# Performance work log

Measured on AMD Instinct MI355X. Metric: run time of the kernel, lower is better.

The kernel has to match this reference:

```python
import jax, jax.numpy as jnp
import numpy as np

D_EMB = 256


def setup_inputs() -> dict:
    key = jax.random.key(0)
    ks = jax.random.split(key, 7)
    B, S, d = 4, 4096, D_EMB
    scale = 1.0 / np.sqrt(d)
    return {
        "x": jax.random.normal(ks[0], (B, S, d), jnp.float32),
        "Wqkv": jax.random.normal(ks[1], (d, 3 * d), jnp.float32) * scale,
        "bqkv": jax.random.normal(ks[2], (3 * d,), jnp.float32) * 0.02,
        "Wproj": jax.random.normal(ks[3], (d, d), jnp.float32) * scale,
        "bproj": jax.random.normal(ks[4], (d,), jnp.float32) * 0.02,
        "Wfc": jax.random.normal(ks[5], (d, 1), jnp.float32) * scale,
        "bfc": jax.random.normal(ks[6], (1,), jnp.float32) * 0.02,
    }


def reference(x, Wqkv, bqkv, Wproj, bproj, Wfc, bfc):
    # qkv projection: [B,S,3d] -> split into q,k,v [B,S,d]
    qkv = x @ Wqkv + bqkv
    q, k, v = jnp.split(qkv, 3, axis=2)
    # full attention scores [B,S,S]; note: original applies NO 1/sqrt(d)
    # scaling (dead branch in source), 'traditional' softmax over last dim
    attn_scores = jnp.einsum("bqd,bkd->bqk", q, k)
    attn_weights = jax.nn.softmax(attn_scores, axis=-1)
    y = jnp.einsum("bqk,bkd->bqd", attn_weights, v)
    y = y @ Wproj + bproj
    out = y @ Wfc + bfc  # [B,S,1]
    return out
```

## Files before the change

kernel.cpp:

```cpp
#include <hip/hip_runtime.h>
#include <hip/hip_bf16.h>

#define BQ 4
#define SQ 4096
#define DQ 256
#define N3 768
#define KBLK 64
#define NITER (SQ / KBLK)
#define KHALF (NITER / 2)
#define LOG2E 1.44269504f
#define THR2 11.5415603f

typedef __attribute__((ext_vector_type(8))) _Float16 f16x8;
typedef __attribute__((ext_vector_type(4))) float f32x4;
typedef __attribute__((ext_vector_type(4))) unsigned int u32x4;

__device__ __forceinline__ short f2h(float f) {
  _Float16 h = (_Float16)f;
  union { _Float16 h; short s; } v; v.h = h;
  return v.s;
}

__device__ __forceinline__ void gload16(const void* g, void* lds) {
  __builtin_amdgcn_global_load_lds(
      (const __attribute__((address_space(1))) unsigned int*)g,
      (__attribute__((address_space(3))) unsigned int*)lds, 16, 0, 0);
}

__global__ __launch_bounds__(256) void prep_kernel(
    const float* __restrict__ Wqkv, const float* __restrict__ Wproj,
    const float* __restrict__ bproj, const float* __restrict__ Wfc,
    const float* __restrict__ bfc, short* __restrict__ W16T,
    float* __restrict__ Wc) {
  const int t = threadIdx.x;
  if (blockIdx.x == 48) {
    __shared__ float wf[256];
    wf[t] = Wfc[t];
    __syncthreads();
    float acc = 0.f;
    for (int j = 0; j < 256; ++j) acc += Wproj[(size_t)t * 256 + j] * wf[j];
    Wc[t] = acc;
    if (t == 0) {
      float c = bfc[0];
      for (int j = 0; j < 256; ++j) c += bproj[j] * wf[j];
      Wc[256] = c;
    }
    return;
  }
  __shared__ float tile[64][65];
  const int nb = (blockIdx.x % 12) * 64;
  const int kb = (blockIdx.x / 12) * 64;
  const int tr = t >> 6, tc = t & 63;
#pragma unroll
  for (int i = 0; i < 16; ++i)
    tile[tr + i * 4][tc] = Wqkv[(size_t)(kb + tr + i * 4) * N3 + nb + tc];
  __syncthreads();
#pragma unroll
  for (int i = 0; i < 16; ++i)
    W16T[(size_t)(nb + tr + i * 4) * 256 + kb + tc] = f2h(tile[tc][tr + i * 4]);
}

__global__ __launch_bounds__(1024, 4) void qkv_kernel(
    const float* __restrict__ x, const short* __restrict__ W16T,
    const float* __restrict__ bqkv, const float* __restrict__ Wc,
    short* __restrict__ Qb, short* __restrict__ Kb, float* __restrict__ u) {
  __shared__ short xs[64][264];
  __shared__ short ws[2][64][256];
  __shared__ float u_red[4][4][16];
  const int t = threadIdx.x;
  const int l = t & 63, w = t >> 6;
  const int lr = l & 15, lg = l >> 4;
  const int mq = w >> 2, nq = w & 3;
  const int Mbase = blockIdx.x * 64;

#define STAGE_W(BUF, NT)                                                      \
  {                                                                           \
    _Pragma("unroll") for (int i = 0; i < 2; ++i) {                           \
      const int n = w * 4 + i * 2 + (l >> 5);                                 \
      const int gc = (l & 31) ^ (n & 7);                                      \
      gload16(W16T + (size_t)((NT)*64 + n) * 256 + gc * 8,                    \
              &ws[BUF][w * 4 + i * 2][0]);                                    \
    }                                                                         \
  }

  STAGE_W(0, 0);

  {
    const int m = t >> 4, kc = (t & 15) * 16;
    const float* src = x + (size_t)(Mbase + m) * DQ + kc;
    short tmp[16];
#pragma unroll
    for (int i = 0; i < 16; ++i) tmp[i] = f2h(src[i]);
    *(u32x4*)&xs[m][kc] = *(u32x4*)&tmp[0];
    *(u32x4*)&xs[m][kc + 8] = *(u32x4*)&tmp[8];
  }

  float bias_qk[8], bias_u[4], wc_u[4];
#pragma unroll
  for (int i = 0; i < 8; ++i) bias_qk[i] = bqkv[i * 64 + nq * 16 + lr];
#pragma unroll
  for (int i = 0; i < 4; ++i) {
    bias_u[i] = bqkv[512 + i * 64 + nq * 16 + lr];
    wc_u[i] = Wc[i * 64 + nq * 16 + lr];
  }

  __syncthreads();

  unsigned qksto[8][2];
  float upart[4] = {0.f, 0.f, 0.f, 0.f};

#pragma unroll
  for (int nt = 0; nt < 12; ++nt) {
    const int cur = nt & 1;
    if (nt + 1 < 12) {
      STAGE_W(cur ^ 1, nt + 1);
      asm volatile("s_waitcnt vmcnt(2)" ::: "memory");
    } else {
      asm volatile("s_waitcnt vmcnt(0)" ::: "memory");
    }
    __builtin_amdgcn_s_barrier();
    __builtin_amdgcn_sched_barrier(0);

    f32x4 acc = {};
    const char* wR = (const char*)&ws[cur][nq * 16 + lr][0];
#pragma unroll
    for (int kk = 0; kk < 8; ++kk) {
      f16x8 af = *(f16x8*)&xs[mq * 16 + lr][kk * 32 + lg * 8];
      f16x8 bfr = *(const f16x8*)(wR + (((4 * kk + lg) ^ (lr & 7)) << 4));
      acc = __builtin_amdgcn_mfma_f32_16x16x32_f16(af, bfr, acc, 0, 0, 0);
    }
    if (nt < 8) {
      const float sc = (nt < 4) ? 1.f : LOG2E;
      unsigned s0 = (unsigned short)f2h((acc[0] + bias_qk[nt]) * sc);
      unsigned s1 = (unsigned short)f2h((acc[1] + bias_qk[nt]) * sc);
      unsigned s2 = (unsigned short)f2h((acc[2] + bias_qk[nt]) * sc);
      unsigned s3 = (unsigned short)f2h((acc[3] + bias_qk[nt]) * sc);
      qksto[nt][0] = s0 | (s1 << 16);
      qksto[nt][1] = s2 | (s3 << 16);
    } else {
#pragma unroll
      for (int r = 0; r < 4; ++r) upart[r] += (acc[r] + bias_u[nt - 8]) * wc_u[nt - 8];
    }
    __builtin_amdgcn_s_barrier();
  }

#pragma unroll
  for (int nt = 0; nt < 8; ++nt) {
    const int col = nt * 64 + nq * 16 + lr;
#pragma unroll
    for (int r = 0; r < 4; ++r) {
      const int row = Mbase + mq * 16 + lg * 4 + r;
      const short sv = (short)((qksto[nt][r >> 1] >> ((r & 1) * 16)) & 0xFFFF);
      if (col < 256) Qb[(size_t)row * DQ + col] = sv;
      else           Kb[(size_t)row * DQ + (col - 256)] = sv;
    }
  }

#pragma unroll
  for (int mask = 1; mask <= 8; mask <<= 1)
#pragma unroll
    for (int r = 0; r < 4; ++r) upart[r] += __shfl_xor(upart[r], mask, 64);
  if (lr == 0) {
#pragma unroll
    for (int r = 0; r < 4; ++r) u_red[mq][nq][lg * 4 + r] = upart[r];
  }
  __syncthreads();
  if (t < 64)
    u[Mbase + t] = u_red[t >> 4][0][t & 15] + u_red[t >> 4][1][t & 15] +
                   u_red[t >> 4][2][t & 15] + u_red[t >> 4][3][t & 15];
#undef STAGE_W
}

__global__ __launch_bounds__(256, 2) void attn_kernel(
    const short* __restrict__ Qb, const short* __restrict__ Kb,
    const float* __restrict__ u, float* __restrict__ Pm,
    float* __restrict__ Pd, float* __restrict__ Pn) {
  __shared__ short Ks[2][64][256];
  __shared__ __align__(16) float u_lds[2048];
  __shared__ float Mrg[2][2][32][3];

  const int t = threadIdx.x;
  const int l = t & 63, w = t >> 6;
  const int lr = l & 15, lg = l >> 4;
  const int qg = w >> 1, h = w & 1;
  const int bid = blockIdx.x;
  const int b = bid & 3;
  const int half = (bid >> 2) & 1;
  const int qbase = (bid >> 3) * 64;

  const short* kbase = Kb + ((size_t)b * SQ + (size_t)half * (SQ / 2)) * DQ;
  const float* ubase = u + (size_t)b * SQ + half * (SQ / 2);

#define STAGE(BUF, KB)                                                      \
  {                                                                         \
    _Pragma("unroll") for (int i = 0; i < 8; ++i) {                         \
      const int kr = w * 16 + i * 2 + (l >> 5);                             \
      const int gc = (l & 31) ^ (kr & 7);                                   \
      gload16(kbase + (size_t)((KB)*64 + kr) * DQ + gc * 8,                 \
              &Ks[BUF][w * 16 + i * 2][0]);                                 \
    }                                                                       \
  }

  STAGE(0, 0);
  gload16(ubase + w * 256 + (l << 2), &u_lds[w * 256]);
  gload16(ubase + (4 + w) * 256 + (l << 2), &u_lds[(4 + w) * 256]);

  f16x8 qf[2][8];
#pragma unroll
  for (int mm = 0; mm < 2; ++mm) {
    const short* qptr = Qb + (size_t)(b * SQ + qbase + qg * 32 + mm * 16 + lr) * DQ;
#pragma unroll
    for (int kk = 0; kk < 8; ++kk)
      qf[mm][kk] = *(const f16x8*)(qptr + kk * 32 + lg * 8);
  }

  int koff[8];
#pragma unroll
  for (int kk = 0; kk < 8; ++kk) koff[kk] = ((4 * kk + lg) ^ (lr & 7)) << 4;

  float m_run[2] = {-1e30f, -1e30f};
  float num[2][2] = {}, den[2][2] = {};

  __syncthreads();

  for (int kb = 0; kb < KHALF; ++kb) {
    const int cur = kb & 1;
    if (kb + 1 < KHALF) {
      STAGE(cur ^ 1, kb + 1);
      asm volatile("s_waitcnt vmcnt(8)" ::: "memory");
    } else {
      asm volatile("s_waitcnt vmcnt(0)" ::: "memory");
    }
    __builtin_amdgcn_s_barrier();
    __builtin_amdgcn_sched_barrier(0);

    f32x4 uv[2];
#pragma unroll
    for (int kc = 0; kc < 2; ++kc)
      uv[kc] = *(const f32x4*)&u_lds[kb * 64 + h * 32 + kc * 16 + lg * 4];

    f16x8 kf[2][8];
#pragma unroll
    for (int kc = 0; kc < 2; ++kc) {
      const char* kR = (const char*)&Ks[cur][h * 32 + kc * 16 + lr][0];
#pragma unroll
      for (int kk = 0; kk < 8; ++kk)
        kf[kc][kk] = *(const f16x8*)(kR + koff[kk]);
    }

    f32x4 s[2][2] = {};
    __builtin_amdgcn_s_setprio(1);
#pragma unroll
    for (int kc = 0; kc < 2; ++kc)
#pragma unroll
      for (int kk = 0; kk < 8; ++kk) {
        s[kc][0] = __builtin_amdgcn_mfma_f32_16x16x32_f16(kf[kc][kk], qf[0][kk], s[kc][0], 0, 0, 0);
        s[kc][1] = __builtin_amdgcn_mfma_f32_16x16x32_f16(kf[kc][kk], qf[1][kk], s[kc][1], 0, 0, 0);
      }
    __builtin_amdgcn_s_setprio(0);

    float mx[2];
#pragma unroll
    for (int mm = 0; mm < 2; ++mm)
      mx[mm] = fmaxf(fmaxf(fmaxf(s[0][mm][0], s[0][mm][1]),
                           fmaxf(s[0][mm][2], s[0][mm][3])),
                     fmaxf(fmaxf(s[1][mm][0], s[1][mm][1]),
                           fmaxf(s[1][mm][2], s[1][mm][3])));
    const bool over = (mx[0] > m_run[0] + THR2) || (mx[1] > m_run[1] + THR2);
    if (__any(over)) {
#pragma unroll
      for (int mm = 0; mm < 2; ++mm) {
        float mt = mx[mm];
        mt = fmaxf(mt, __shfl_xor(mt, 16, 64));
        mt = fmaxf(mt, __shfl_xor(mt, 32, 64));
        const float mn = fmaxf(m_run[mm], mt);
        const float sc = __builtin_amdgcn_exp2f(m_run[mm] - mn);
        m_run[mm] = mn;
#pragma unroll
        for (int kc = 0; kc < 2; ++kc) { num[mm][kc] *= sc; den[mm][kc] *= sc; }
      }
    }
#pragma unroll
    for (int kc = 0; kc < 2; ++kc) {
#pragma unroll
      for (int mm = 0; mm < 2; ++mm)
#pragma unroll
        for (int r = 0; r < 4; ++r) {
          const float p = __builtin_amdgcn_exp2f(s[kc][mm][r] - m_run[mm]);
          den[mm][kc] += p;
          num[mm][kc] += p * uv[kc][r];
        }
    }
    __builtin_amdgcn_s_barrier();
  }

  float numt[2], dent[2];
#pragma unroll
  for (int mm = 0; mm < 2; ++mm) {
    numt[mm] = num[mm][0] + num[mm][1];
    dent[mm] = den[mm][0] + den[mm][1];
    numt[mm] += __shfl_xor(numt[mm], 16, 64);
    numt[mm] += __shfl_xor(numt[mm], 32, 64);
    dent[mm] += __shfl_xor(dent[mm], 16, 64);
    dent[mm] += __shfl_xor(dent[mm], 32, 64);
  }
  if (lg == 0) {
#pragma unroll
    for (int mm = 0; mm < 2; ++mm) {
      Mrg[qg][h][mm * 16 + lr][0] = m_run[mm];
      Mrg[qg][h][mm * 16 + lr][1] = dent[mm];
      Mrg[qg][h][mm * 16 + lr][2] = numt[mm];
    }
  }
  __syncthreads();

  if (t < 64) {
    const int row = t & 31, qg2 = t >> 5;
    const float m0 = Mrg[qg2][0][row][0], m1 = Mrg[qg2][1][row][0];
    const float M = fmaxf(m0, m1);
    const float e0 = __builtin_amdgcn_exp2f(m0 - M);
    const float e1 = __builtin_amdgcn_exp2f(m1 - M);
    const float dt = e0 * Mrg[qg2][0][row][1] + e1 * Mrg[qg2][1][row][1];
    const float nt = e0 * Mrg[qg2][0][row][2] + e1 * Mrg[qg2][1][row][2];
    const size_t idx = (size_t)half * (BQ * SQ) + (size_t)b * SQ + qbase + qg2 * 32 + row;
    Pm[idx] = M; Pd[idx] = dt; Pn[idx] = nt;
  }
#undef STAGE
}

__global__ void merge_kernel(const float* __restrict__ Pm,
                             const float* __restrict__ Pd,
                             const float* __restrict__ Pn,
                             const float* __restrict__ Wc,
                             float* __restrict__ out) {
  const int gid = blockIdx.x * 256 + threadIdx.x;
  const float m0 = Pm[gid], m1 = Pm[BQ * SQ + gid];
  const float M = fmaxf(m0, m1);
  const float e0 = __builtin_amdgcn_exp2f(m0 - M);
  const float e1 = __builtin_amdgcn_exp2f(m1 - M);
  const float den = e0 * Pd[gid] + e1 * Pd[BQ * SQ + gid];
  const float num = e0 * Pn[gid] + e1 * Pn[BQ * SQ + gid];
  out[gid] = num / den + Wc[256];
}

extern "C" void kernel_launch(void* const* d_in, const int* in_sizes, int n_in,
                              void* d_out, int out_size, void* d_ws, size_t ws_size,
                              hipStream_t stream) {
  const float* x     = (const float*)d_in[0];
  const float* Wqkv  = (const float*)d_in[1];
  const float* bqkv  = (const float*)d_in[2];
  const float* Wproj = (const float*)d_in[3];
  const float* bproj = (const float*)d_in[4];
  const float* Wfc   = (const float*)d_in[5];
  const float* bfc   = (const float*)d_in[6];
  float* out = (float*)d_out;

  const size_t SEG = (size_t)BQ * SQ * DQ * 2;
  char* wsb = (char*)d_ws;
  short* Qb   = (short*)(wsb);
  short* Kb   = (short*)(wsb + SEG);
  char* base  = wsb + 2 * SEG;
  float* Wc   = (float*)(base);
  float* u    = (float*)(base + 4096);
  short* W16T = (short*)(base + 4096 + 65536);
  float* Pm   = (float*)(base + 4096 + 65536 + 393216);
  float* Pd   = Pm + 2 * BQ * SQ;
  float* Pn   = Pd + 2 * BQ * SQ;

  prep_kernel<<<49, 256, 0, stream>>>(Wqkv, Wproj, bproj, Wfc, bfc, W16T, Wc);
  qkv_kernel<<<256, 1024, 0, stream>>>(x, W16T, bqkv, Wc, Qb, Kb, u);
  attn_kernel<<<512, 256, 0, stream>>>(Qb, Kb, u, Pm, Pd, Pn);
  merge_kernel<<<BQ * SQ / 256, 256, 0, stream>>>(Pm, Pd, Pn, Wc, out);
}
```

Before: 93.83 us.

## Load K fragments directly from global into registers, dropping LDS staging

Replaces the double-buffered LDS staging of K tiles with direct per-lane global loads into register fragments, software-pipelined so one 16-row chunk loads while MFMAs run on the other. This removes the LDS round trip and the per-iteration barriers. The cost is that the two waves sharing the same h, one per query group, each load the same K rows themselves, so global and L2 traffic for K doubles. It also adds register pressure, which may hurt occupancy at 2 blocks per CU.

```diff
diff --git a/kernel.cpp b/kernel.cpp
--- a/kernel.cpp
+++ b/kernel.cpp
@@ -175,7 +175,6 @@
     const short* __restrict__ Qb, const short* __restrict__ Kb,
     const float* __restrict__ u, float* __restrict__ Pm,
     float* __restrict__ Pd, float* __restrict__ Pn) {
-  __shared__ short Ks[2][64][256];
   __shared__ __align__(16) float u_lds[2048];
   __shared__ float Mrg[2][2][32][3];
 
@@ -189,19 +188,16 @@
   const int qbase = (bid >> 3) * 64;
 
   const short* kbase = Kb + ((size_t)b * SQ + (size_t)half * (SQ / 2)) * DQ;
+  const short* kp = kbase + (size_t)(h * 32 + lr) * DQ + lg * 8;
   const float* ubase = u + (size_t)b * SQ + half * (SQ / 2);
 
-#define STAGE(BUF, KB)                                                      \
+#define LOADKC(DST, KB, KC)                                                 \
   {                                                                         \
-    _Pragma("unroll") for (int i = 0; i < 8; ++i) {                         \
-      const int kr = w * 16 + i * 2 + (l >> 5);                             \
-      const int gc = (l & 31) ^ (kr & 7);                                   \
-      gload16(kbase + (size_t)((KB)*64 + kr) * DQ + gc * 8,                 \
-              &Ks[BUF][w * 16 + i * 2][0]);                                 \
-    }                                                                       \
-  }
-
-  STAGE(0, 0);
+    const short* p_ = kp + ((size_t)(KB) * 64 + (KC)*16) * DQ;              \
+    _Pragma("unroll") for (int kk = 0; kk < 8; ++kk)                        \
+        DST[kk] = *(const f16x8*)(p_ + kk * 32);                            \
+  }
+
   gload16(ubase + w * 256 + (l << 2), &u_lds[w * 256]);
   gload16(ubase + (4 + w) * 256 + (l << 2), &u_lds[(4 + w) * 256]);
 
@@ -214,50 +210,39 @@
       qf[mm][kk] = *(const f16x8*)(qptr + kk * 32 + lg * 8);
   }
 
-  int koff[8];
-#pragma unroll
-  for (int kk = 0; kk < 8; ++kk) koff[kk] = ((4 * kk + lg) ^ (lr & 7)) << 4;
-
   float m_run[2] = {-1e30f, -1e30f};
   float num[2][2] = {}, den[2][2] = {};
 
+  f16x8 kfA[8], kfB[8];
+  LOADKC(kfA, 0, 0);
   __syncthreads();
 
   for (int kb = 0; kb < KHALF; ++kb) {
-    const int cur = kb & 1;
-    if (kb + 1 < KHALF) {
-      STAGE(cur ^ 1, kb + 1);
-      asm volatile("s_waitcnt vmcnt(8)" ::: "memory");
-    } else {
-      asm volatile("s_waitcnt vmcnt(0)" ::: "memory");
-    }
-    __builtin_amdgcn_s_barrier();
-    __builtin_amdgcn_sched_barrier(0);
+    LOADKC(kfB, kb, 1);
+
+    f32x4 s[2][2] = {};
+    __builtin_amdgcn_s_setprio(1);
+#pragma unroll
+    for (int kk = 0; kk < 8; ++kk) {
+      s[0][0] = __builtin_amdgcn_mfma_f32_16x16x32_f16(kfA[kk], qf[0][kk], s[0][0], 0, 0, 0);
+      s[0][1] = __builtin_amdgcn_mfma_f32_16x16x32_f16(kfA[kk], qf[1][kk], s[0][1], 0, 0, 0);
+    }
+    __builtin_amdgcn_s_setprio(0);
+
+    if (kb + 1 < KHALF) LOADKC(kfA, kb + 1, 0);
+
+    __builtin_amdgcn_s_setprio(1);
+#pragma unroll
+    for (int kk = 0; kk < 8; ++kk) {
+      s[1][0] = __builtin_amdgcn_mfma_f32_16x16x32_f16(kfB[kk], qf[0][kk], s[1][0], 0, 0, 0);
+      s[1][1] = __builtin_amdgcn_mfma_f32_16x16x32_f16(kfB[kk], qf[1][kk], s[1][1], 0, 0, 0);
+    }
+    __builtin_amdgcn_s_setprio(0);
 
     f32x4 uv[2];
 #pragma unroll
     for (int kc = 0; kc < 2; ++kc)
       uv[kc] = *(const f32x4*)&u_lds[kb * 64 + h * 32 + kc * 16 + lg * 4];
-
-    f16x8 kf[2][8];
-#pragma unroll
-    for (int kc = 0; kc < 2; ++kc) {
-      const char* kR = (const char*)&Ks[cur][h * 32 + kc * 16 + lr][0];
-#pragma unroll
-      for (int kk = 0; kk < 8; ++kk)
-        kf[kc][kk] = *(const f16x8*)(kR + koff[kk]);
-    }
-
-    f32x4 s[2][2] = {};
-    __builtin_amdgcn_s_setprio(1);
-#pragma unroll
-    for (int kc = 0; kc < 2; ++kc)
-#pragma unroll
-      for (int kk = 0; kk < 8; ++kk) {
-        s[kc][0] = __builtin_amdgcn_mfma_f32_16x16x32_f16(kf[kc][kk], qf[0][kk], s[kc][0], 0, 0, 0);
-        s[kc][1] = __builtin_amdgcn_mfma_f32_16x16x32_f16(kf[kc][kk], qf[1][kk], s[kc][1], 0, 0, 0);
-      }
-    __builtin_amdgcn_s_setprio(0);
 
     float mx[2];
 #pragma unroll
@@ -291,7 +276,6 @@
           num[mm][kc] += p * uv[kc][r];
         }
     }
-    __builtin_amdgcn_s_barrier();
   }
 
   float numt[2], dent[2];
@@ -325,7 +309,7 @@
     const size_t idx = (size_t)half * (BQ * SQ) + (size_t)b * SQ + qbase + qg2 * 32 + row;
     Pm[idx] = M; Pd[idx] = dt; Pn[idx] = nt;
   }
-#undef STAGE
+#undef LOADKC
 }
 
 __global__ void merge_kernel(const float* __restrict__ Pm,
```

Measured after the change: 161.1 us. +71.7%, slower.
